# Kernel tuning notes

Hardware: AMD Instinct MI355X
Metric: run time of the kernel (lower is better)

The kernel has to match this reference:

```python
import jax, jax.numpy as jnp
import numpy as np

NUM_BUCKETS = 32
MAX_DISTANCE = 128
NUM_HEADS = 16
D_KV = 64


def _relative_position_bucket(relative_position):
    # bidirectional buckets, faithful to T5Attention._relative_position_bucket
    num_buckets = NUM_BUCKETS // 2
    relative_buckets = (relative_position > 0).astype(jnp.int32) * num_buckets
    relative_position = jnp.abs(relative_position)
    max_exact = num_buckets // 2
    is_small = relative_position < max_exact
    rp_f = relative_position.astype(jnp.float32)
    rel_if_large = max_exact + (
        jnp.log(rp_f / max_exact) / np.log(MAX_DISTANCE / max_exact) * (num_buckets - max_exact)
    )
    rel_if_large = jnp.minimum(rel_if_large, num_buckets - 1)
    relative_buckets = relative_buckets + jnp.where(is_small, rp_f, rel_if_large).astype(jnp.int32)
    return relative_buckets


def setup_inputs() -> dict:
    key = jax.random.key(0)
    ks = jax.random.split(key, 6)
    B, S, D = 2, 2048, 1024
    inner = NUM_HEADS * D_KV  # 1024
    q_std = (inner * D_KV) ** (-0.5)
    kv_std = inner ** (-0.5)
    return {
        "hidden_states": jax.random.normal(ks[0], (B, S, D), jnp.float32),
        "attention_mask": jnp.ones((B, S), jnp.int32),
        "Wq": jax.random.normal(ks[1], (D, inner), jnp.float32) * q_std,
        "Wk": jax.random.normal(ks[2], (D, inner), jnp.float32) * kv_std,
        "Wv": jax.random.normal(ks[3], (D, inner), jnp.float32) * kv_std,
        "Wo": jax.random.normal(ks[4], (inner, D), jnp.float32) * kv_std,
        "rel_bias": jax.random.normal(ks[5], (NUM_BUCKETS, NUM_HEADS), jnp.float32),
    }


def reference(hidden_states, attention_mask, Wq, Wk, Wv, Wo, rel_bias):
    B, S, D = hidden_states.shape
    H, Dk = NUM_HEADS, D_KV

    q = (hidden_states @ Wq).reshape(B, S, H, Dk)
    k = (hidden_states @ Wk).reshape(B, S, H, Dk)
    v = (hidden_states @ Wv).reshape(B, S, H, Dk)
    q = q / jnp.sqrt(jnp.asarray(Dk, q.dtype))

    scores = jnp.einsum('bthd,bshd->bhts', q, k)  # [B,H,S,S]

    # relative position bias
    pos = jnp.arange(S, dtype=jnp.int32)
    rel_pos = pos[None, :] - pos[:, None]          # memory - context, [S,S]
    buckets = _relative_position_bucket(rel_pos)   # [S,S]
    bias = rel_bias[buckets]                       # [S,S,H]
    scores = scores + bias.transpose(2, 0, 1)[None].astype(scores.dtype)

    mask = attention_mask[:, None, None, :].astype(scores.dtype)
    scores = scores + (1.0 - mask) * jnp.finfo(scores.dtype).min

    attn = jax.nn.softmax(scores, axis=-1)
    out = jnp.einsum('bhts,bshd->bthd', attn, v).reshape(B, S, H * Dk)
    return out @ Wo
```

## Files before the change

kernel.cpp:

```cpp
#include <hip/hip_runtime.h>
#include <hip/hip_bf16.h>
#include <math.h>

typedef __attribute__((ext_vector_type(8))) short bf16x8;
typedef __attribute__((ext_vector_type(4))) short s16x4;
typedef __attribute__((ext_vector_type(4))) float f32x4;

constexpr int cB = 2, cS = 2048, cH = 16, cD = 64, cIn = 1024, cM = 1024;
constexpr float cLog2e = 1.4426950408889634f;

union BfPack { bf16x8 v; short s[8]; };
union BfPack4 { s16x4 v; short s[4]; };

__device__ __forceinline__ short f2bf(float f) {
    union { float f; unsigned u; } v; v.f = f;
    unsigned r = v.u + 0x7fffu + ((v.u >> 16) & 1u);
    return (short)(r >> 16);
}

__device__ __forceinline__ f32x4 mfma16(bf16x8 a, bf16x8 b, f32x4 c) {
    return __builtin_amdgcn_mfma_f32_16x16x32_bf16(a, b, c, 0, 0, 0);
}

__device__ __forceinline__ void async16(const short* g, short* l) {
    __builtin_amdgcn_global_load_lds(
        (const __attribute__((address_space(1))) unsigned*)(uintptr_t)g,
        (__attribute__((address_space(3))) unsigned*)(uintptr_t)l, 16, 0, 0);
}

__global__ void bias_table_kernel(const float* __restrict__ rel_bias,
                                  const int* __restrict__ mask,
                                  float* __restrict__ bt,
                                  float* __restrict__ maskadd) {
    int idx = blockIdx.x * blockDim.x + threadIdx.x;
    if (idx < 4096) maskadd[idx] = (1.0f - (float)mask[idx]) * -3.0e38f;
    if (idx >= 4095) return;
    int delta = idx - 2047;
    int rb = (delta > 0) ? 16 : 0;
    int ar = delta < 0 ? -delta : delta;
    int bucket;
    if (ar < 8) {
        bucket = rb + ar;
    } else {
        float rl = 8.0f + logf((float)ar * 0.125f) * 2.8853900817779268f;
        rl = fminf(rl, 15.0f);
        bucket = rb + (int)rl;
    }
    #pragma unroll
    for (int h = 0; h < cH; h++)
        bt[h * 4096 + 2048 + delta] = rel_bias[bucket * cH + h] * cLog2e;
}

__global__ __launch_bounds__(256) void conv_hidden_kernel(
    const float* __restrict__ h, short* __restrict__ hbf) {
    int t = blockIdx.x * 256 + threadIdx.x;
    const float4* src = (const float4*)h;
    float4 a = src[2 * t], b = src[2 * t + 1];
    BfPack p;
    p.s[0] = f2bf(a.x); p.s[1] = f2bf(a.y); p.s[2] = f2bf(a.z); p.s[3] = f2bf(a.w);
    p.s[4] = f2bf(b.x); p.s[5] = f2bf(b.y); p.s[6] = f2bf(b.z); p.s[7] = f2bf(b.w);
    ((bf16x8*)hbf)[t] = p.v;
}

__global__ __launch_bounds__(256) void conv_wt_kernel(
    const float* __restrict__ Wq, const float* __restrict__ Wk,
    const float* __restrict__ Wv, const float* __restrict__ Wo,
    short* __restrict__ Wt) {
    const int z = blockIdx.z;
    const float* W = (z == 0) ? Wq : (z == 1) ? Wk : (z == 2) ? Wv : Wo;
    const float scale = (z == 0) ? 0.125f * cLog2e : 1.0f;
    const int n0 = blockIdx.x * 64, k0 = blockIdx.y * 64;
    __shared__ short sW[64][72];
    const int t = threadIdx.x;
    const int r = t >> 2, c4 = (t & 3) * 16;
    {
        const float* src = W + (size_t)(k0 + r) * cM + n0 + c4;
        BfPack p[2];
        #pragma unroll
        for (int q = 0; q < 2; q++) {
            float4 x = ((const float4*)src)[2 * q];
            float4 y = ((const float4*)src)[2 * q + 1];
            p[q].s[0] = f2bf(x.x * scale); p[q].s[1] = f2bf(x.y * scale);
            p[q].s[2] = f2bf(x.z * scale); p[q].s[3] = f2bf(x.w * scale);
            p[q].s[4] = f2bf(y.x * scale); p[q].s[5] = f2bf(y.y * scale);
            p[q].s[6] = f2bf(y.z * scale); p[q].s[7] = f2bf(y.w * scale);
        }
        *(bf16x8*)&sW[r][c4] = p[0].v;
        *(bf16x8*)&sW[r][c4 + 8] = p[1].v;
    }
    __syncthreads();
    const int n = t >> 2, kc = (t & 3) * 16;
    BfPack o0, o1;
    #pragma unroll
    for (int j = 0; j < 8; j++) o0.s[j] = sW[kc + j][n];
    #pragma unroll
    for (int j = 0; j < 8; j++) o1.s[j] = sW[kc + 8 + j][n];
    short* dst = Wt + (size_t)z * cM * cIn + (size_t)(n0 + n) * cIn + k0 + kc;
    *(bf16x8*)dst = o0.v;
    *(bf16x8*)(dst + 8) = o1.v;
}

template <bool SWAP>
__device__ __forceinline__ void gemm_core(
    const short* __restrict__ A, const short* __restrict__ Bt,
    short* smem, int m0, int c0, int tid, f32x4 (&acc)[4][4]) {
    short* sA = smem;
    short* sB = smem + 4096;
    const int w = tid >> 6, l = tid & 63;
    const int m16 = l & 15, g = l >> 4;
    const int srow = l >> 2, scol = (l & 3) * 8;
    const int mq = (w & 1) * 64, nq = (w >> 1) * 64;

    for (int k0 = 0; k0 < cIn; k0 += 32) {
        __syncthreads();
        async16(A + (size_t)(m0 + w * 16 + srow) * cIn + k0 + scol,
                sA + w * 512 + l * 8);
        async16(A + (size_t)(m0 + 64 + w * 16 + srow) * cIn + k0 + scol,
                sA + 2048 + w * 512 + l * 8);
        async16(Bt + (size_t)(c0 + w * 16 + srow) * cIn + k0 + scol,
                sB + w * 512 + l * 8);
        async16(Bt + (size_t)(c0 + 64 + w * 16 + srow) * cIn + k0 + scol,
                sB + 2048 + w * 512 + l * 8);
        __syncthreads();
        bf16x8 af[4], bf[4];
        #pragma unroll
        for (int i = 0; i < 4; i++)
            af[i] = *(const bf16x8*)(sA + (mq + i * 16 + m16) * 32 + g * 8);
        #pragma unroll
        for (int j = 0; j < 4; j++)
            bf[j] = *(const bf16x8*)(sB + (nq + j * 16 + m16) * 32 + g * 8);
        #pragma unroll
        for (int i = 0; i < 4; i++)
            #pragma unroll
            for (int j = 0; j < 4; j++)
                acc[i][j] = SWAP ? mfma16(bf[j], af[i], acc[i][j])
                                 : mfma16(af[i], bf[j], acc[i][j]);
    }
}

__global__ __launch_bounds__(256) void gemm_qkv_kernel(
    const short* __restrict__ hbf, const short* __restrict__ Wt,
    short* __restrict__ Qrm, short* __restrict__ Krm, short* __restrict__ VT) {
    const int z = blockIdx.z;
    const short* Bt = Wt + (size_t)z * cM * cIn;
    const int m0 = blockIdx.y * 128, c0 = blockIdx.x * 128;
    __shared__ short smem[8192];
    const int tid = threadIdx.x, w = tid >> 6, l = tid & 63;
    const int m16 = l & 15, g = l >> 4;
    const int mq = (w & 1) * 64, nq = (w >> 1) * 64;
    f32x4 acc[4][4] = {};

    if (z <= 1) {
        gemm_core<false>(hbf, Bt, smem, m0, c0, tid, acc);
        short* dst = (z == 0) ? Qrm : Krm;
        #pragma unroll
        for (int i = 0; i < 4; i++)
            #pragma unroll
            for (int j = 0; j < 4; j++)
                #pragma unroll
                for (int r = 0; r < 4; r++)
                    dst[(size_t)(m0 + mq + i * 16 + g * 4 + r) * cM +
                        c0 + nq + j * 16 + m16] = f2bf(acc[i][j][r]);
    } else {
        gemm_core<true>(hbf, Bt, smem, m0, c0, tid, acc);
        #pragma unroll
        for (int i = 0; i < 4; i++) {
            const int srow_g = m0 + mq + i * 16 + m16;
            const int bb = srow_g >> 11, ss = srow_g & 2047;
            const int s6 = ss & 63;
            const int kap = (s6 & 3) | ((s6 & 28) << 1) | ((s6 >> 3) & 4);
            const int col = (ss & ~63) + kap;
            #pragma unroll
            for (int j = 0; j < 4; j++)
                #pragma unroll
                for (int r = 0; r < 4; r++) {
                    const int wcol = c0 + nq + j * 16 + g * 4 + r;
                    VT[(((size_t)bb * cH + (wcol >> 6)) * cD + (wcol & 63)) * cS
                       + col] = f2bf(acc[i][j][r]);
                }
        }
    }
}

__global__ __launch_bounds__(256, 2) void attn_kernel(
    const short* __restrict__ Qrm, const short* __restrict__ Krm,
    const short* __restrict__ VTK, const float* __restrict__ maskadd,
    const float* __restrict__ bias_t, short* __restrict__ ctx) {
    const int b = blockIdx.z, h = blockIdx.y;
    const int q0 = blockIdx.x * 128;
    const short* VTp = VTK + ((size_t)b * cH + h) * cS * cD;
    const float* bh = bias_t + h * 4096 + 2048;
    const float* mp = maskadd + b * cS;

    const int tid = threadIdx.x;
    const int wave = tid >> 6, lane = tid & 63;
    const int m16 = lane & 15, g = lane >> 4;

    __shared__ short Kt[2][128 * 64];
    __shared__ short Vt[2][64 * 128];

    int qv[2];
    bf16x8 qf[2][2];
    #pragma unroll
    for (int qq = 0; qq < 2; qq++) {
        qv[qq] = q0 + qq * 64 + wave * 16 + m16;
        const short* qb = Qrm + (size_t)(b * cS + qv[qq]) * cM + h * cD;
        qf[qq][0] = *(const bf16x8*)(qb + g * 8);
        qf[qq][1] = *(const bf16x8*)(qb + 32 + g * 8);
    }

    f32x4 o[2][4] = {};
    f32x4 lacc[2] = {};
    BfPack ones;
    #pragma unroll
    for (int i = 0; i < 8; i++) ones.s[i] = (short)0x3F80;

    const int u8 = tid & 7, r8 = tid >> 3;
    const int u16s = tid & 15, r16 = tid >> 4;
    const short* pK = Krm + ((size_t)b * cS + r8) * cM + h * cD +
                      ((u8 ^ (r8 & 7)) << 3);
    const short* pV = VTp + (size_t)r16 * cS + ((u16s ^ (r16 & 7)) << 3);
    short* dK = (short*)Kt + tid * 8;
    short* dV = (short*)Vt + tid * 8;

    const int kx0 = ((g ^ (m16 & 7)) << 3);
    const int kx1 = (((g + 4) ^ (m16 & 7)) << 3);

    #pragma unroll
    for (int c = 0; c < 4; c++) {
        async16(pK + (size_t)(c * 32) * cM, dK + c * 2048);
        async16(pV + (size_t)(c * 16) * cS, dV + c * 2048);
    }
    __syncthreads();

    for (int kt = 0; kt < cS; kt += 128) {
        const int buf = (kt >> 7) & 1, nxt = buf ^ 1;
        if (kt + 128 < cS) {
            #pragma unroll
            for (int c = 0; c < 4; c++) {
                async16(pK + (size_t)(kt + 128 + c * 32) * cM,
                        dK + nxt * 8192 + c * 2048);
                async16(pV + (size_t)(c * 16) * cS + kt + 128,
                        dV + nxt * 8192 + c * 2048);
            }
        }
        const short* K_ = (const short*)Kt + buf * 8192;
        const short* V_ = (const short*)Vt + buf * 8192;

        #pragma unroll
        for (int h2 = 0; h2 < 2; h2++) {
            f32x4 s[2][4];
            __builtin_amdgcn_s_setprio(1);
            #pragma unroll
            for (int t4 = 0; t4 < 4; t4++) {
                const int st = h2 * 4 + t4;
                const int keyb = kt + st * 16 + g * 4;
                bf16x8 klo = *(const bf16x8*)(K_ + (st * 16 + m16) * 64 + kx0);
                bf16x8 khi = *(const bf16x8*)(K_ + (st * 16 + m16) * 64 + kx1);
                #pragma unroll
                for (int qq = 0; qq < 2; qq++) {
                    f32x4 init;
                    #pragma unroll
                    for (int c = 0; c < 4; c++)
                        init[c] = bh[keyb + c - qv[qq]] + mp[keyb + c];
                    s[qq][t4] = mfma16(khi, qf[qq][1],
                                       mfma16(klo, qf[qq][0], init));
                }
            }
            __builtin_amdgcn_s_setprio(0);

            BfPack pp[2][2];
            #pragma unroll
            for (int qq = 0; qq < 2; qq++)
                #pragma unroll
                for (int t4 = 0; t4 < 4; t4++)
                    #pragma unroll
                    for (int r = 0; r < 2; r++) {
                        float p0 = __builtin_amdgcn_exp2f(s[qq][t4][2 * r]);
                        float p1 = __builtin_amdgcn_exp2f(s[qq][t4][2 * r + 1]);
                        __hip_bfloat162 h2v = __float22bfloat162_rn(float2{p0, p1});
                        short2 sp = *(short2*)&h2v;
                        pp[qq][t4 & 1].s[(t4 >> 1) * 4 + 2 * r]     = sp.x;
                        pp[qq][t4 & 1].s[(t4 >> 1) * 4 + 2 * r + 1] = sp.y;
                    }

            __builtin_amdgcn_s_setprio(1);
            #pragma unroll
            for (int qq = 0; qq < 2; qq++) {
                lacc[qq] = mfma16(ones.v, pp[qq][0].v, lacc[qq]);
                lacc[qq] = mfma16(ones.v, pp[qq][1].v, lacc[qq]);
            }
            #pragma unroll
            for (int nt = 0; nt < 4; nt++) {
                bf16x8 vlo = *(const bf16x8*)(V_ + (nt * 16 + m16) * 128 +
                                              h2 * 64 + kx0);
                bf16x8 vhi = *(const bf16x8*)(V_ + (nt * 16 + m16) * 128 +
                                              h2 * 64 + kx1);
                #pragma unroll
                for (int qq = 0; qq < 2; qq++) {
                    o[qq][nt] = mfma16(vlo, pp[qq][0].v, o[qq][nt]);
                    o[qq][nt] = mfma16(vhi, pp[qq][1].v, o[qq][nt]);
                }
            }
            __builtin_amdgcn_s_setprio(0);
        }

        __syncthreads();
    }

    #pragma unroll
    for (int qq = 0; qq < 2; qq++) {
        const float inv = 1.0f / lacc[qq][0];
        short* cb = ctx + (size_t)(b * cS + qv[qq]) * cM + h * cD;
        #pragma unroll
        for (int nt = 0; nt < 4; nt++) {
            BfPack4 pk;
            #pragma unroll
            for (int r = 0; r < 4; r++) pk.s[r] = f2bf(o[qq][nt][r] * inv);
            *(s16x4*)(cb + nt * 16 + g * 4) = pk.v;
        }
    }
}

__global__ __launch_bounds__(256) void gemm_o_kernel(
    const short* __restrict__ ctx, const short* __restrict__ WoT,
    float* __restrict__ out) {
    const int m0 = blockIdx.y * 128, c0 = blockIdx.x * 128;
    __shared__ short smem[8192];
    const int tid = threadIdx.x, w = tid >> 6, l = tid & 63;
    const int m16 = l & 15, g = l >> 4;
    const int mq = (w & 1) * 64, nq = (w >> 1) * 64;
    f32x4 acc[4][4] = {};
    gemm_core<false>(ctx, WoT, smem, m0, c0, tid, acc);
    #pragma unroll
    for (int i = 0; i < 4; i++)
        #pragma unroll
        for (int j = 0; j < 4; j++)
            #pragma unroll
            for (int r = 0; r < 4; r++)
                out[(size_t)(m0 + mq + i * 16 + g * 4 + r) * cM +
                    c0 + nq + j * 16 + m16] = acc[i][j][r];
}

extern "C" void kernel_launch(void* const* d_in, const int* in_sizes, int n_in,
                              void* d_out, int out_size, void* d_ws, size_t ws_size,
                              hipStream_t stream) {
    const float* hidden   = (const float*)d_in[0];
    const int*   mask     = (const int*)d_in[1];
    const float* Wq       = (const float*)d_in[2];
    const float* Wk       = (const float*)d_in[3];
    const float* Wv       = (const float*)d_in[4];
    const float* Wo       = (const float*)d_in[5];
    const float* rel_bias = (const float*)d_in[6];
    float* out = (float*)d_out;

    short* hbf_ctx = (short*)d_ws;
    short* Wt  = hbf_ctx + (size_t)4 * 1024 * 1024;
    short* Qrm = Wt  + (size_t)4 * 1024 * 1024;
    short* Krm = Qrm + (size_t)4 * 1024 * 1024;
    short* VT  = Krm + (size_t)4 * 1024 * 1024;
    float* bias_t  = (float*)(VT + (size_t)4 * 1024 * 1024);
    float* maskf   = bias_t + 16 * 4096;

    bias_table_kernel<<<16, 256, 0, stream>>>(rel_bias, mask, bias_t, maskf);
    conv_hidden_kernel<<<2048, 256, 0, stream>>>(hidden, hbf_ctx);
    conv_wt_kernel<<<dim3(16, 16, 4), 256, 0, stream>>>(Wq, Wk, Wv, Wo, Wt);
    gemm_qkv_kernel<<<dim3(8, 32, 3), 256, 0, stream>>>(hbf_ctx, Wt, Qrm, Krm, VT);
    attn_kernel<<<dim3(16, cH, cB), 256, 0, stream>>>(Qrm, Krm, VT, maskf, bias_t,
                                                      hbf_ctx);
    gemm_o_kernel<<<dim3(8, 32), 256, 0, stream>>>(hbf_ctx, Wt + (size_t)3 * 1024 * 1024,
                                                   out);
}
```

Baseline: 222.6 us.

## Split attention over key halves, stage QKV epilogue stores through shared memory

The attention kernel can now split the key range into two halves across extra blocks, with a new combine kernel that merges the partial outputs and row sums. Key tiles shrink to 64 with smaller shared buffers, and the launch bound rises to 4 blocks per CU. The QKV GEMM epilogue now transposes through padded shared memory so global stores are coalesced 16-byte writes instead of scattered 2-byte ones. The split path only runs when the workspace is large enough, and it adds fp32 partial-result traffic plus an extra launch.

```diff
diff --git a/kernel.cpp b/kernel.cpp
--- a/kernel.cpp
+++ b/kernel.cpp
@@ -144,7 +144,7 @@
     const int z = blockIdx.z;
     const short* Bt = Wt + (size_t)z * cM * cIn;
     const int m0 = blockIdx.y * 128, c0 = blockIdx.x * 128;
-    __shared__ short smem[8192];
+    __shared__ short smem[128 * 132];
     const int tid = threadIdx.x, w = tid >> 6, l = tid & 63;
     const int m16 = l & 15, g = l >> 4;
     const int mq = (w & 1) * 64, nq = (w >> 1) * 64;
@@ -152,41 +152,58 @@
 
     if (z <= 1) {
         gemm_core<false>(hbf, Bt, smem, m0, c0, tid, acc);
-        short* dst = (z == 0) ? Qrm : Krm;
+        __syncthreads();
         #pragma unroll
         for (int i = 0; i < 4; i++)
             #pragma unroll
             for (int j = 0; j < 4; j++)
                 #pragma unroll
                 for (int r = 0; r < 4; r++)
-                    dst[(size_t)(m0 + mq + i * 16 + g * 4 + r) * cM +
-                        c0 + nq + j * 16 + m16] = f2bf(acc[i][j][r]);
+                    smem[(mq + i * 16 + g * 4 + r) * 132 + nq + j * 16 + m16] =
+                        f2bf(acc[i][j][r]);
+        __syncthreads();
+        const int tr = tid >> 1, hf = (tid & 1) * 64;
+        short* dst = ((z == 0) ? Qrm : Krm) + (size_t)(m0 + tr) * cM + c0 + hf;
+        #pragma unroll
+        for (int c = 0; c < 8; c++)
+            *(bf16x8*)(dst + c * 8) = *(const bf16x8*)(smem + tr * 132 + hf + c * 8);
     } else {
         gemm_core<true>(hbf, Bt, smem, m0, c0, tid, acc);
+        __syncthreads();
         #pragma unroll
         for (int i = 0; i < 4; i++) {
-            const int srow_g = m0 + mq + i * 16 + m16;
-            const int bb = srow_g >> 11, ss = srow_g & 2047;
-            const int s6 = ss & 63;
-            const int kap = (s6 & 3) | ((s6 & 28) << 1) | ((s6 >> 3) & 4);
-            const int col = (ss & ~63) + kap;
+            const int sl = mq + i * 16 + m16;
+            const int s6 = sl & 63;
+            const int pcol = (sl & 64) +
+                             ((s6 & 3) | ((s6 & 28) << 1) | ((s6 >> 3) & 4));
             #pragma unroll
             for (int j = 0; j < 4; j++)
                 #pragma unroll
-                for (int r = 0; r < 4; r++) {
-                    const int wcol = c0 + nq + j * 16 + g * 4 + r;
-                    VT[(((size_t)bb * cH + (wcol >> 6)) * cD + (wcol & 63)) * cS
-                       + col] = f2bf(acc[i][j][r]);
-                }
-        }
-    }
-}
-
-__global__ __launch_bounds__(256, 2) void attn_kernel(
+                for (int r = 0; r < 4; r++)
+                    smem[(nq + j * 16 + g * 4 + r) * 132 + pcol] =
+                        f2bf(acc[i][j][r]);
+        }
+        __syncthreads();
+        const int tr = tid >> 1, hf = (tid & 1) * 64;
+        const int wcol = c0 + tr;
+        short* dst = VT + (((size_t)(m0 >> 11) * cH + (wcol >> 6)) * cD +
+                           (wcol & 63)) * cS + (m0 & 2047) + hf;
+        #pragma unroll
+        for (int c = 0; c < 8; c++)
+            *(bf16x8*)(dst + c * 8) = *(const bf16x8*)(smem + tr * 132 + hf + c * 8);
+    }
+}
+
+__global__ __launch_bounds__(256, 4) void attn_kernel(
     const short* __restrict__ Qrm, const short* __restrict__ Krm,
     const short* __restrict__ VTK, const float* __restrict__ maskadd,
-    const float* __restrict__ bias_t, short* __restrict__ ctx) {
-    const int b = blockIdx.z, h = blockIdx.y;
+    const float* __restrict__ bias_t, short* __restrict__ ctx,
+    float* __restrict__ op, float* __restrict__ lp) {
+    const int nsplit = gridDim.z / cB;
+    const int b = blockIdx.z / nsplit, kh = blockIdx.z % nsplit;
+    const int KEYS = cS / nsplit;
+    const int k0 = kh * KEYS;
+    const int h = blockIdx.y;
     const int q0 = blockIdx.x * 128;
     const short* VTp = VTK + ((size_t)b * cH + h) * cS * cD;
     const float* bh = bias_t + h * 4096 + 2048;
@@ -196,8 +213,8 @@
     const int wave = tid >> 6, lane = tid & 63;
     const int m16 = lane & 15, g = lane >> 4;
 
-    __shared__ short Kt[2][128 * 64];
-    __shared__ short Vt[2][64 * 128];
+    __shared__ short Kt[2][64 * 64];
+    __shared__ short Vt[2][64 * 64];
 
     int qv[2];
     bf16x8 qf[2][2];
@@ -215,110 +232,143 @@
     #pragma unroll
     for (int i = 0; i < 8; i++) ones.s[i] = (short)0x3F80;
 
-    const int u8 = tid & 7, r8 = tid >> 3;
-    const int u16s = tid & 15, r16 = tid >> 4;
-    const short* pK = Krm + ((size_t)b * cS + r8) * cM + h * cD +
-                      ((u8 ^ (r8 & 7)) << 3);
-    const short* pV = VTp + (size_t)r16 * cS + ((u16s ^ (r16 & 7)) << 3);
+    const int r2 = tid >> 3, u = tid & 7;
+    const short* srcK = Krm + ((size_t)b * cS + k0 + r2) * cM + h * cD +
+                        ((u ^ (r2 & 7)) << 3);
+    const short* srcV = VTp + (size_t)r2 * cS + k0 + ((u ^ (r2 & 7)) << 3);
     short* dK = (short*)Kt + tid * 8;
     short* dV = (short*)Vt + tid * 8;
 
     const int kx0 = ((g ^ (m16 & 7)) << 3);
     const int kx1 = (((g + 4) ^ (m16 & 7)) << 3);
 
-    #pragma unroll
-    for (int c = 0; c < 4; c++) {
-        async16(pK + (size_t)(c * 32) * cM, dK + c * 2048);
-        async16(pV + (size_t)(c * 16) * cS, dV + c * 2048);
-    }
+    async16(srcK, dK);
+    async16(srcK + (size_t)32 * cM, dK + 2048);
+    async16(srcV, dV);
+    async16(srcV + (size_t)32 * cS, dV + 2048);
     __syncthreads();
 
-    for (int kt = 0; kt < cS; kt += 128) {
-        const int buf = (kt >> 7) & 1, nxt = buf ^ 1;
-        if (kt + 128 < cS) {
-            #pragma unroll
-            for (int c = 0; c < 4; c++) {
-                async16(pK + (size_t)(kt + 128 + c * 32) * cM,
-                        dK + nxt * 8192 + c * 2048);
-                async16(pV + (size_t)(c * 16) * cS + kt + 128,
-                        dV + nxt * 8192 + c * 2048);
-            }
-        }
-        const short* K_ = (const short*)Kt + buf * 8192;
-        const short* V_ = (const short*)Vt + buf * 8192;
-
-        #pragma unroll
-        for (int h2 = 0; h2 < 2; h2++) {
-            f32x4 s[2][4];
-            __builtin_amdgcn_s_setprio(1);
-            #pragma unroll
-            for (int t4 = 0; t4 < 4; t4++) {
-                const int st = h2 * 4 + t4;
-                const int keyb = kt + st * 16 + g * 4;
-                bf16x8 klo = *(const bf16x8*)(K_ + (st * 16 + m16) * 64 + kx0);
-                bf16x8 khi = *(const bf16x8*)(K_ + (st * 16 + m16) * 64 + kx1);
-                #pragma unroll
-                for (int qq = 0; qq < 2; qq++) {
-                    f32x4 init;
-                    #pragma unroll
-                    for (int c = 0; c < 4; c++)
-                        init[c] = bh[keyb + c - qv[qq]] + mp[keyb + c];
-                    s[qq][t4] = mfma16(khi, qf[qq][1],
-                                       mfma16(klo, qf[qq][0], init));
-                }
-            }
-            __builtin_amdgcn_s_setprio(0);
-
-            BfPack pp[2][2];
+    const int ntiles = KEYS >> 6;
+    for (int t = 0; t < ntiles; t++) {
+        const int buf = t & 1, nxt = buf ^ 1;
+        if (t + 1 < ntiles) {
+            const size_t ko = (size_t)(t + 1) * 64;
+            async16(srcK + ko * cM, dK + nxt * 4096);
+            async16(srcK + (ko + 32) * cM, dK + nxt * 4096 + 2048);
+            async16(srcV + ko, dV + nxt * 4096);
+            async16(srcV + (size_t)32 * cS + ko, dV + nxt * 4096 + 2048);
+        }
+        const short* K_ = (const short*)Kt + buf * 4096;
+        const short* V_ = (const short*)Vt + buf * 4096;
+        const int kt = k0 + t * 64;
+
+        f32x4 init[2][4];
+        #pragma unroll
+        for (int st = 0; st < 4; st++) {
+            const int keyb = kt + st * 16 + g * 4;
             #pragma unroll
             for (int qq = 0; qq < 2; qq++)
                 #pragma unroll
-                for (int t4 = 0; t4 < 4; t4++)
-                    #pragma unroll
-                    for (int r = 0; r < 2; r++) {
-                        float p0 = __builtin_amdgcn_exp2f(s[qq][t4][2 * r]);
-                        float p1 = __builtin_amdgcn_exp2f(s[qq][t4][2 * r + 1]);
-                        __hip_bfloat162 h2v = __float22bfloat162_rn(float2{p0, p1});
-                        short2 sp = *(short2*)&h2v;
-                        pp[qq][t4 & 1].s[(t4 >> 1) * 4 + 2 * r]     = sp.x;
-                        pp[qq][t4 & 1].s[(t4 >> 1) * 4 + 2 * r + 1] = sp.y;
-                    }
-
-            __builtin_amdgcn_s_setprio(1);
+                for (int c = 0; c < 4; c++)
+                    init[qq][st][c] = bh[keyb + c - qv[qq]] + mp[keyb + c];
+        }
+
+        f32x4 s[2][4];
+        __builtin_amdgcn_s_setprio(1);
+        #pragma unroll
+        for (int st = 0; st < 4; st++) {
+            bf16x8 klo = *(const bf16x8*)(K_ + (st * 16 + m16) * 64 + kx0);
+            bf16x8 khi = *(const bf16x8*)(K_ + (st * 16 + m16) * 64 + kx1);
+            #pragma unroll
+            for (int qq = 0; qq < 2; qq++)
+                s[qq][st] = mfma16(khi, qf[qq][1],
+                                   mfma16(klo, qf[qq][0], init[qq][st]));
+        }
+        __builtin_amdgcn_s_setprio(0);
+
+        BfPack pp[2][2];
+        #pragma unroll
+        for (int qq = 0; qq < 2; qq++)
+            #pragma unroll
+            for (int st = 0; st < 4; st++)
+                #pragma unroll
+                for (int r = 0; r < 2; r++) {
+                    float p0 = __builtin_amdgcn_exp2f(s[qq][st][2 * r]);
+                    float p1 = __builtin_amdgcn_exp2f(s[qq][st][2 * r + 1]);
+                    __hip_bfloat162 h2v = __float22bfloat162_rn(float2{p0, p1});
+                    short2 sp = *(short2*)&h2v;
+                    pp[qq][st & 1].s[(st >> 1) * 4 + 2 * r]     = sp.x;
+                    pp[qq][st & 1].s[(st >> 1) * 4 + 2 * r + 1] = sp.y;
+                }
+
+        __builtin_amdgcn_s_setprio(1);
+        #pragma unroll
+        for (int qq = 0; qq < 2; qq++) {
+            lacc[qq] = mfma16(ones.v, pp[qq][0].v, lacc[qq]);
+            lacc[qq] = mfma16(ones.v, pp[qq][1].v, lacc[qq]);
+        }
+        #pragma unroll
+        for (int nt = 0; nt < 4; nt++) {
+            bf16x8 vlo = *(const bf16x8*)(V_ + (nt * 16 + m16) * 64 + kx0);
+            bf16x8 vhi = *(const bf16x8*)(V_ + (nt * 16 + m16) * 64 + kx1);
             #pragma unroll
             for (int qq = 0; qq < 2; qq++) {
-                lacc[qq] = mfma16(ones.v, pp[qq][0].v, lacc[qq]);
-                lacc[qq] = mfma16(ones.v, pp[qq][1].v, lacc[qq]);
+                o[qq][nt] = mfma16(vlo, pp[qq][0].v, o[qq][nt]);
+                o[qq][nt] = mfma16(vhi, pp[qq][1].v, o[qq][nt]);
             }
+        }
+        __builtin_amdgcn_s_setprio(0);
+
+        __syncthreads();
+    }
+
+    if (nsplit == 1) {
+        #pragma unroll
+        for (int qq = 0; qq < 2; qq++) {
+            const float inv = 1.0f / lacc[qq][0];
+            short* cb = ctx + (size_t)(b * cS + qv[qq]) * cM + h * cD;
             #pragma unroll
             for (int nt = 0; nt < 4; nt++) {
-                bf16x8 vlo = *(const bf16x8*)(V_ + (nt * 16 + m16) * 128 +
-                                              h2 * 64 + kx0);
-                bf16x8 vhi = *(const bf16x8*)(V_ + (nt * 16 + m16) * 128 +
-                                              h2 * 64 + kx1);
+                BfPack4 pk;
                 #pragma unroll
-                for (int qq = 0; qq < 2; qq++) {
-                    o[qq][nt] = mfma16(vlo, pp[qq][0].v, o[qq][nt]);
-                    o[qq][nt] = mfma16(vhi, pp[qq][1].v, o[qq][nt]);
-                }
+                for (int r = 0; r < 4; r++) pk.s[r] = f2bf(o[qq][nt][r] * inv);
+                *(s16x4*)(cb + nt * 16 + g * 4) = pk.v;
             }
-            __builtin_amdgcn_s_setprio(0);
-        }
-
-        __syncthreads();
-    }
-
-    #pragma unroll
-    for (int qq = 0; qq < 2; qq++) {
-        const float inv = 1.0f / lacc[qq][0];
-        short* cb = ctx + (size_t)(b * cS + qv[qq]) * cM + h * cD;
-        #pragma unroll
-        for (int nt = 0; nt < 4; nt++) {
-            BfPack4 pk;
-            #pragma unroll
-            for (int r = 0; r < 4; r++) pk.s[r] = f2bf(o[qq][nt][r] * inv);
-            *(s16x4*)(cb + nt * 16 + g * 4) = pk.v;
-        }
+        }
+    } else {
+        #pragma unroll
+        for (int qq = 0; qq < 2; qq++) {
+            float* ob = op + ((((size_t)(kh * cB + b)) * cH + h) * cS + qv[qq]) * cD;
+            #pragma unroll
+            for (int nt = 0; nt < 4; nt++)
+                *(f32x4*)(ob + nt * 16 + g * 4) = o[qq][nt];
+            if (g == 0)
+                lp[(((size_t)(kh * cB + b)) * cH + h) * cS + qv[qq]] = lacc[qq][0];
+        }
+    }
+}
+
+__global__ __launch_bounds__(256) void combine_kernel(
+    const float* __restrict__ op, const float* __restrict__ lp,
+    short* __restrict__ ctx) {
+    const int t = blockIdx.x * 256 + threadIdx.x;
+    const int quarter = t & 3, row = t >> 2;
+    const int q = row & 2047, h = (row >> 11) & 15, b = row >> 15;
+    const size_t r0 = ((size_t)b * cH + h) * cS + q;
+    const size_t r1 = ((size_t)(cB + b) * cH + h) * cS + q;
+    const float inv = 1.0f / (lp[r0] + lp[r1]);
+    const float4* p0 = (const float4*)(op + r0 * cD + quarter * 16);
+    const float4* p1 = (const float4*)(op + r1 * cD + quarter * 16);
+    short* dst = ctx + ((size_t)b * cS + q) * cM + h * cD + quarter * 16;
+    #pragma unroll
+    for (int c = 0; c < 4; c++) {
+        float4 a = p0[c], d4 = p1[c];
+        BfPack4 pk;
+        pk.s[0] = f2bf((a.x + d4.x) * inv);
+        pk.s[1] = f2bf((a.y + d4.y) * inv);
+        pk.s[2] = f2bf((a.z + d4.z) * inv);
+        pk.s[3] = f2bf((a.w + d4.w) * inv);
+        *(s16x4*)(dst + c * 4) = pk.v;
     }
 }
 
@@ -361,13 +411,19 @@
     short* VT  = Krm + (size_t)4 * 1024 * 1024;
     float* bias_t  = (float*)(VT + (size_t)4 * 1024 * 1024);
     float* maskf   = bias_t + 16 * 4096;
+    float* op      = maskf + 4096;
+    float* lp      = op + (size_t)2 * cB * cH * cS * cD;
+
+    const int nsplit = (ws_size >= (size_t)76 * 1024 * 1024) ? 2 : 1;
 
     bias_table_kernel<<<16, 256, 0, stream>>>(rel_bias, mask, bias_t, maskf);
     conv_hidden_kernel<<<2048, 256, 0, stream>>>(hidden, hbf_ctx);
     conv_wt_kernel<<<dim3(16, 16, 4), 256, 0, stream>>>(Wq, Wk, Wv, Wo, Wt);
     gemm_qkv_kernel<<<dim3(8, 32, 3), 256, 0, stream>>>(hbf_ctx, Wt, Qrm, Krm, VT);
-    attn_kernel<<<dim3(16, cH, cB), 256, 0, stream>>>(Qrm, Krm, VT, maskf, bias_t,
-                                                      hbf_ctx);
+    attn_kernel<<<dim3(16, cH, cB * nsplit), 256, 0, stream>>>(
+        Qrm, Krm, VT, maskf, bias_t, hbf_ctx, op, lp);
+    if (nsplit == 2)
+        combine_kernel<<<1024, 256, 0, stream>>>(op, lp, hbf_ctx);
     gemm_o_kernel<<<dim3(8, 32), 256, 0, stream>>>(hbf_ctx, Wt + (size_t)3 * 1024 * 1024,
                                                    out);
 }
```

After: 230.3 us. 1.03x slower.
